# Kernel tuning notes

Hardware: AMD Instinct MI355X
Metric: run time of the kernel (lower is better)

The kernel has to match this reference:

```python
import jax, jax.numpy as jnp
import numpy as np

B, CIN, COUT, HID, K, H, W = 16, 512, 512, 512, 3, 64, 64

def setup_inputs() -> dict:
    key = jax.random.key(0)
    ks = jax.random.split(key, 8)
    x = jax.random.normal(ks[0], (B, CIN, H, W), dtype=jnp.float32)
    y = jax.random.normal(ks[1], (B, HID), dtype=jnp.float32)
    noise = jax.random.normal(ks[2], (B, 1, H, W), dtype=jnp.float32)
    # params (lrmul=1): weight ~ N(0,1)/sqrt(lrmul), bias zeros
    weight = jax.random.normal(ks[3], (COUT, CIN, K, K), dtype=jnp.float32)
    bias = jnp.zeros((1, COUT, 1, 1), dtype=jnp.float32)
    # ScaleLinear (equalized-lr linear): raw weight ~ N(0,1), runtime scale 1/sqrt(fan_in)
    mod_w = jax.random.normal(ks[4], (CIN, HID), dtype=jnp.float32)
    mod_b = jnp.zeros((CIN,), dtype=jnp.float32)
    noise_scale = jnp.zeros((1,), dtype=jnp.float32)
    return {"x": x, "y": y, "noise": noise, "weight": weight, "bias": bias,
            "mod_w": mod_w, "mod_b": mod_b, "noise_scale": noise_scale}

def reference(x, y, noise, weight, bias, mod_w, mod_b, noise_scale):
    O, I, k, _ = weight.shape
    runtime_coef = 1.0 / np.sqrt(I * k * k)  # gain=1, lrmul=1
    w = weight * runtime_coef                # shared scaled weight [O,I,k,k]
    # style modulation: s = mod(y) + 1, equalized-lr linear scale 1/sqrt(hidden)
    mod_scale = 1.0 / np.sqrt(mod_w.shape[1])
    s = y @ (mod_w.T * mod_scale) + mod_b + 1.0   # [B, I]
    # demodulation coeff without materializing per-sample weights:
    # d[b,o] = rsqrt(sum_{i,kx,ky} (w[o,i]*s[b,i])^2 + eps)
    w2 = jnp.sum(w * w, axis=(2, 3))              # [O, I]
    d = jax.lax.rsqrt(jnp.einsum('oi,bi->bo', w2, s * s) + 1e-8)  # [B, O]
    # fold modulation into input scale, demod into output scale (StyleGAN2 trick;
    # mathematically identical to grouped conv with per-sample weights)
    xm = x * s[:, :, None, None]
    out = jax.lax.conv_general_dilated(
        xm, w, window_strides=(1, 1), padding=((1, 1), (1, 1)),
        dimension_numbers=('NCHW', 'OIHW', 'NCHW'))
    out = out * d[:, :, None, None]
    out = out + noise * noise_scale   # noisy=True, explicit noise input
    out = out + bias                  # lrmul=1
    return out
```

## Files before the change

### kernel.cpp

```cpp
#include <hip/hip_runtime.h>
#include <hip/hip_bf16.h>

typedef unsigned short ushortT;
typedef __attribute__((ext_vector_type(8))) short short8;
typedef __attribute__((ext_vector_type(4))) float f32x4;

#define CIN 512
#define COUTC 512
#define HIDC 512
#define BATCH 16
#define HDIM 64
#define WDIM 64
#define HP 66


__device__ __forceinline__ unsigned short f2bf(float f) {
    __hip_bfloat16 h = __float2bfloat16(f);
    return __builtin_bit_cast(unsigned short, h);
}

__device__ __forceinline__ void gload16(const ushortT* g, ushortT* l) {
    __builtin_amdgcn_global_load_lds(
        (const __attribute__((address_space(1))) void*)g,
        (__attribute__((address_space(3))) void*)l, 16, 0, 0);
}

__global__ void k_style(const float* __restrict__ y, const float* __restrict__ mw,
                        const float* __restrict__ mb, float* __restrict__ s) {
    int lane = threadIdx.x & 63;
    int wid = blockIdx.x * 4 + (threadIdx.x >> 6);
    int b = wid >> 9, i = wid & 511;
    int h0 = lane * 8;
    float4 ya = *(const float4*)(y + b * HIDC + h0);
    float4 yb = *(const float4*)(y + b * HIDC + h0 + 4);
    float4 wa = *(const float4*)(mw + (size_t)i * HIDC + h0);
    float4 wb = *(const float4*)(mw + (size_t)i * HIDC + h0 + 4);
    float v = ya.x*wa.x + ya.y*wa.y + ya.z*wa.z + ya.w*wa.w
            + yb.x*wb.x + yb.y*wb.y + yb.z*wb.z + yb.w*wb.w;
    #pragma unroll
    for (int off = 32; off > 0; off >>= 1) v += __shfl_down(v, off);
    if (lane == 0) s[wid] = v * 0.04419417382415922f + mb[i] + 1.0f;
}

__global__ void k_prepw(const float* __restrict__ w, float* __restrict__ w2,
                        ushortT* __restrict__ wbt) {
    int t = blockIdx.x * 256 + threadIdx.x;
    const float* wp = w + (size_t)t * 9;
    const float coef = 0.014731391274719739f;
    float sum = 0.f;
    #pragma unroll
    for (int k = 0; k < 9; ++k) {
        float v = wp[k] * coef;
        sum += v * v;
        wbt[(size_t)k * (COUTC * CIN) + t] = f2bf(v);
    }
    w2[t] = sum;
}

__global__ void k_demod(const float* __restrict__ w2, const float* __restrict__ s,
                        float* __restrict__ d) {
    int lane = threadIdx.x & 63;
    int wid = blockIdx.x * 4 + (threadIdx.x >> 6);
    int b = wid >> 9, o = wid & 511;
    int i0 = lane * 8;
    float4 wa = *(const float4*)(w2 + (size_t)o * CIN + i0);
    float4 wb = *(const float4*)(w2 + (size_t)o * CIN + i0 + 4);
    float4 sa = *(const float4*)(s + b * CIN + i0);
    float4 sb = *(const float4*)(s + b * CIN + i0 + 4);
    float v = wa.x*sa.x*sa.x + wa.y*sa.y*sa.y + wa.z*sa.z*sa.z + wa.w*sa.w*sa.w
            + wb.x*sb.x*sb.x + wb.y*sb.y*sb.y + wb.z*sb.z*sb.z + wb.w*sb.w*sb.w;
    #pragma unroll
    for (int off = 32; off > 0; off >>= 1) v += __shfl_down(v, off);
    if (lane == 0) d[wid] = rsqrtf(v + 1e-8f);
}

__global__ void k_pad(const float* __restrict__ x, const float* __restrict__ s,
                      ushortT* __restrict__ xpad) {
    __shared__ float tilef[64 * 129];
    int bid = blockIdx.x;
    int cchunk = bid & 3;
    int rem = bid >> 2;
    int prow = rem % HP;
    int b = rem / HP;
    int tid = threadIdx.x;
    size_t rowbase = (((size_t)b * HP + prow) * HP) * CIN + cchunk * 128;
    if (prow == 0 || prow == HP - 1) {
        short8 z = {};
        for (int q = tid; q < HP * 16; q += 256) {
            int col = q >> 4, sub = q & 15;
            *(short8*)(xpad + rowbase + (size_t)col * CIN + sub * 8) = z;
        }
        return;
    }
    int xr = prow - 1;
    int u = tid & 15;
    int cbase = tid >> 4;
    #pragma unroll
    for (int it = 0; it < 8; ++it) {
        int c = cbase + it * 16;
        int ch = cchunk * 128 + c;
        float4 v = *(const float4*)(x + (((size_t)b * CIN + ch) * HDIM + xr) * WDIM + u * 4);
        float sv = s[b * CIN + ch];
        tilef[(u * 4 + 0) * 129 + c] = v.x * sv;
        tilef[(u * 4 + 1) * 129 + c] = v.y * sv;
        tilef[(u * 4 + 2) * 129 + c] = v.z * sv;
        tilef[(u * 4 + 3) * 129 + c] = v.w * sv;
    }
    __syncthreads();
    #pragma unroll
    for (int it = 0; it < 4; ++it) {
        int q = it * 256 + tid;
        int col = 1 + (q >> 4);
        int sub = q & 15;
        const float* tr = tilef + (col - 1) * 129 + sub * 8;
        short8 o;
        #pragma unroll
        for (int r = 0; r < 8; ++r) o[r] = (short)f2bf(tr[r]);
        *(short8*)(xpad + rowbase + (size_t)col * CIN + sub * 8) = o;
    }
    if (tid < 32) {
        short8 z = {};
        int bcol = (tid < 16) ? 0 : (HP - 1);
        *(short8*)(xpad + rowbase + (size_t)bcol * CIN + (tid & 15) * 8) = z;
    }
}

#define MFMA_CLUSTER(MH) do { \
    __builtin_amdgcn_s_setprio(1); \
    _Pragma("unroll") for (int m_ = 0; m_ < 4; ++m_) { \
        _Pragma("unroll") for (int n_ = 0; n_ < 4; ++n_) \
            acc[(MH)*4 + m_][n_] = __builtin_amdgcn_mfma_f32_16x16x32_bf16( \
                af[m_], bf[n_], acc[(MH)*4 + m_][n_], 0, 0, 0); } \
    __builtin_amdgcn_s_setprio(0); \
} while (0)

#define DS_A(MH, KH) do { \
    _Pragma("unroll") for (int m_ = 0; m_ < 4; ++m_) { \
        int row_ = wave_m * 128 + (MH)*64 + m_*16 + l15; \
        af[m_] = *(const short8*)(Ar + row_*64 + ((((KH)*4 + quad) ^ (row_ & 7)) * 8)); \
    } } while (0)

#define DS_B(KH) do { \
    _Pragma("unroll") for (int n_ = 0; n_ < 4; ++n_) { \
        int row_ = wave_n * 64 + n_*16 + l15; \
        bf[n_] = *(const short8*)(Br + row_*64 + ((((KH)*4 + quad) ^ (row_ & 7)) * 8)); \
    } } while (0)

__global__ __launch_bounds__(512, 2) void k_conv(
    const ushortT* __restrict__ wbt, const ushortT* __restrict__ xpad,
    const float* __restrict__ dcoef, const float* __restrict__ bias,
    const float* __restrict__ noise, const float* __restrict__ nscp,
    float* __restrict__ out)
{
    extern __shared__ __align__(16) ushortT smem[];

    int tid = threadIdx.x;
    int lane = tid & 63;
    int wave = tid >> 6;
    int wave_m = wave >> 2;
    int wave_n = wave & 3;
    int l15 = lane & 15;
    int quad = lane >> 4;

    int bid = blockIdx.x;
    int wg = (bid & 7) * 64 + (bid >> 3);
    int mtile = wg >> 8;
    int ntile = wg & 255;
    int b = ntile >> 4;
    int h0 = (ntile & 15) << 2;
    int cout0 = mtile << 8;

    unsigned aoff[4], boff[4], dstE[4];
    #pragma unroll
    for (int ca = 0; ca < 4; ++ca) {
        int a = ca * 512 + tid;
        int row = a >> 3;
        int sub = (a & 7) ^ (row & 7);
        aoff[ca] = (unsigned)((cout0 + row) * CIN + sub * 8);
        int prow = row >> 6;
        int pcol = row & 63;
        boff[ca] = (unsigned)((((b * HP) + h0 + prow) * HP + pcol) * CIN + sub * 8);
        dstE[ca] = (unsigned)(ca * 4096 + wave * 512);
    }

    f32x4 acc[8][4] = {};

    {
        const ushortT* Asrc = wbt;
        const ushortT* Bsrc = xpad;
        #pragma unroll
        for (int ca = 0; ca < 4; ++ca) {
            gload16(Asrc + aoff[ca], smem + dstE[ca]);
            gload16(Bsrc + boff[ca], smem + 32768 + dstE[ca]);
        }
        asm volatile("s_waitcnt vmcnt(0)" ::: "memory");
        __builtin_amdgcn_s_barrier();
    }

    #pragma unroll 2
    for (int ks = 0; ks < 72; ++ks) {
        int cur = ks & 1;
        const ushortT* Ar = smem + cur * 16384;
        const ushortT* Br = smem + 32768 + cur * 16384;
        ushortT* Aw = smem + (cur ^ 1) * 16384;
        ushortT* Bw = smem + 32768 + (cur ^ 1) * 16384;
        int ksn = ks + 1;
        bool st = ksn < 72;
        int tn = ksn >> 3, ccn = ksn & 7;
        const ushortT* Asrc = wbt + tn * (COUTC * CIN) + ccn * 64;
        const ushortT* Bsrc = xpad + ((tn / 3) * HP + (tn % 3)) * CIN + ccn * 64;

        short8 af[4], bf[4];

        if (st) {
            gload16(Asrc + aoff[0], Aw + dstE[0]); gload16(Bsrc + boff[0], Bw + dstE[0]);
            gload16(Asrc + aoff[1], Aw + dstE[1]); gload16(Bsrc + boff[1], Bw + dstE[1]);
        }
        DS_B(0);
        DS_A(0, 0);
        __builtin_amdgcn_s_barrier();
        asm volatile("s_waitcnt lgkmcnt(0)");
        MFMA_CLUSTER(0);
        __builtin_amdgcn_s_barrier();

        if (st) {
            gload16(Asrc + aoff[2], Aw + dstE[2]); gload16(Bsrc + boff[2], Bw + dstE[2]);
            gload16(Asrc + aoff[3], Aw + dstE[3]); gload16(Bsrc + boff[3], Bw + dstE[3]);
        }
        DS_A(1, 0);
        __builtin_amdgcn_s_barrier();
        asm volatile("s_waitcnt lgkmcnt(0)");
        MFMA_CLUSTER(1);
        __builtin_amdgcn_s_barrier();

        DS_B(1);
        DS_A(0, 1);
        __builtin_amdgcn_s_barrier();
        asm volatile("s_waitcnt lgkmcnt(0)");
        MFMA_CLUSTER(0);
        __builtin_amdgcn_s_barrier();

        DS_A(1, 1);
        __builtin_amdgcn_s_barrier();
        asm volatile("s_waitcnt lgkmcnt(0)");
        MFMA_CLUSTER(1);
        if (st) asm volatile("s_waitcnt vmcnt(0)");
        __builtin_amdgcn_s_barrier();
    }

    float ns = nscp[0];
    int col = lane & 15, rq = lane >> 4;
    #pragma unroll
    for (int nj = 0; nj < 4; ++nj) {
        int pos = wave_n * 64 + nj * 16 + col;
        int hh = h0 + (pos >> 6), ww = pos & 63;
        float nz = noise[((size_t)b << 12) + (hh << 6) + ww] * ns;
        #pragma unroll
        for (int mi = 0; mi < 8; ++mi) {
            int coutb = cout0 + wave_m * 128 + mi * 16 + rq * 4;
            f32x4 dv = *(const f32x4*)(dcoef + b * COUTC + coutb);
            f32x4 bv = *(const f32x4*)(bias + coutb);
            f32x4 a = acc[mi][nj];
            #pragma unroll
            for (int r = 0; r < 4; ++r) {
                out[(((size_t)(b * COUTC + coutb + r)) << 12) + (hh << 6) + ww]
                    = a[r] * dv[r] + nz + bv[r];
            }
        }
    }
}

extern "C" void kernel_launch(void* const* d_in, const int* in_sizes, int n_in,
                              void* d_out, int out_size, void* d_ws, size_t ws_size,
                              hipStream_t stream) {
    const float* x      = (const float*)d_in[0];
    const float* y      = (const float*)d_in[1];
    const float* noise  = (const float*)d_in[2];
    const float* weight = (const float*)d_in[3];
    const float* bias   = (const float*)d_in[4];
    const float* mod_w  = (const float*)d_in[5];
    const float* mod_b  = (const float*)d_in[6];
    const float* nsc    = (const float*)d_in[7];
    float* out = (float*)d_out;

    char* ws = (char*)d_ws;
    float*   s     = (float*)(ws);
    float*   dcoef = (float*)(ws + 32768);
    float*   w2    = (float*)(ws + 65536);
    ushortT* wbt   = (ushortT*)(ws + 1114112);
    ushortT* xpad  = (ushortT*)(ws + 5832704);

    static bool attr_done = false;
    if (!attr_done) {
        (void)hipFuncSetAttribute(reinterpret_cast<const void*>(k_conv),
                                  hipFuncAttributeMaxDynamicSharedMemorySize, 131072);
        attr_done = true;
    }

    k_style<<<dim3(2048), dim3(256), 0, stream>>>(y, mod_w, mod_b, s);
    k_prepw<<<dim3(1024), dim3(256), 0, stream>>>(weight, w2, wbt);
    k_demod<<<dim3(2048), dim3(256), 0, stream>>>(w2, s, dcoef);
    k_pad<<<dim3(BATCH * HP * 4), dim3(256), 0, stream>>>(x, s, xpad);
    k_conv<<<dim3(512), dim3(512), 131072, stream>>>(wbt, xpad, dcoef, bias, noise, nsc, out);
}
```

Measured before the change: 532.7 us.

## Switch conv main loop to 4-stage pipeline with BK=32 and deeper prefetch

```diff
diff --git a/kernel.cpp b/kernel.cpp
--- a/kernel.cpp
+++ b/kernel.cpp
@@ -12,6 +12,7 @@
 #define HDIM 64
 #define WDIM 64
 #define HP 66
+#define NSTEP 144
 
 
 __device__ __forceinline__ unsigned short f2bf(float f) {
@@ -125,7 +126,7 @@
     }
 }
 
-#define MFMA_CLUSTER(MH) do { \
+#define CLUST(MH) do { \
     __builtin_amdgcn_s_setprio(1); \
     _Pragma("unroll") for (int m_ = 0; m_ < 4; ++m_) { \
         _Pragma("unroll") for (int n_ = 0; n_ < 4; ++n_) \
@@ -134,17 +135,29 @@
     __builtin_amdgcn_s_setprio(0); \
 } while (0)
 
-#define DS_A(MH, KH) do { \
+#define DS_A(MH, Abase) do { \
     _Pragma("unroll") for (int m_ = 0; m_ < 4; ++m_) { \
         int row_ = wave_m * 128 + (MH)*64 + m_*16 + l15; \
-        af[m_] = *(const short8*)(Ar + row_*64 + ((((KH)*4 + quad) ^ (row_ & 7)) * 8)); \
+        af[m_] = *(const short8*)((Abase) + row_*32 + ((quad ^ ((row_ >> 2) & 3)) * 8)); \
     } } while (0)
 
-#define DS_B(KH) do { \
+#define DS_B(Bbase) do { \
     _Pragma("unroll") for (int n_ = 0; n_ < 4; ++n_) { \
         int row_ = wave_n * 64 + n_*16 + l15; \
-        bf[n_] = *(const short8*)(Br + row_*64 + ((((KH)*4 + quad) ^ (row_ & 7)) * 8)); \
+        bf[n_] = *(const short8*)((Bbase) + row_*32 + ((quad ^ ((row_ >> 2) & 3)) * 8)); \
     } } while (0)
+
+#define STAGE(KSN) do { \
+    int tn_ = (KSN) >> 4, ccn_ = (KSN) & 15; \
+    const ushortT* As_ = wbt + (size_t)tn_ * (COUTC * CIN) + ccn_ * 32; \
+    const ushortT* Bs_ = xpad + ((size_t)(tn_ / 3) * HP + (tn_ % 3)) * CIN + ccn_ * 32; \
+    ushortT* Ad_ = smem + ((KSN) & 3) * 8192; \
+    ushortT* Bd_ = smem + 32768 + ((KSN) & 3) * 8192; \
+    gload16(As_ + aoff[0], Ad_ + dstE[0]); \
+    gload16(As_ + aoff[1], Ad_ + dstE[1]); \
+    gload16(Bs_ + boff[0], Bd_ + dstE[0]); \
+    gload16(Bs_ + boff[1], Bd_ + dstE[1]); \
+} while (0)
 
 __global__ __launch_bounds__(512, 2) void k_conv(
     const ushortT* __restrict__ wbt, const ushortT* __restrict__ xpad,
@@ -170,12 +183,12 @@
     int h0 = (ntile & 15) << 2;
     int cout0 = mtile << 8;
 
-    unsigned aoff[4], boff[4], dstE[4];
-    #pragma unroll
-    for (int ca = 0; ca < 4; ++ca) {
+    unsigned aoff[2], boff[2], dstE[2];
+    #pragma unroll
+    for (int ca = 0; ca < 2; ++ca) {
         int a = ca * 512 + tid;
-        int row = a >> 3;
-        int sub = (a & 7) ^ (row & 7);
+        int row = a >> 2;
+        int sub = (a & 3) ^ ((row >> 2) & 3);
         aoff[ca] = (unsigned)((cout0 + row) * CIN + sub * 8);
         int prow = row >> 6;
         int pcol = row & 63;
@@ -185,67 +198,39 @@
 
     f32x4 acc[8][4] = {};
 
-    {
-        const ushortT* Asrc = wbt;
-        const ushortT* Bsrc = xpad;
-        #pragma unroll
-        for (int ca = 0; ca < 4; ++ca) {
-            gload16(Asrc + aoff[ca], smem + dstE[ca]);
-            gload16(Bsrc + boff[ca], smem + 32768 + dstE[ca]);
+    STAGE(0);
+    STAGE(1);
+    STAGE(2);
+    asm volatile("s_waitcnt vmcnt(8)" ::: "memory");
+    __builtin_amdgcn_s_barrier();
+
+    #pragma unroll 4
+    for (int ks = 0; ks < NSTEP; ++ks) {
+        int buf = ks & 3;
+        const ushortT* Abuf = smem + buf * 8192;
+        const ushortT* Bbuf = smem + 32768 + buf * 8192;
+        int ksn = ks + 3;
+
+        short8 af[4], bf[4];
+
+        if (ksn < NSTEP) STAGE(ksn);
+        DS_B(Bbuf);
+        DS_A(0, Abuf);
+        __builtin_amdgcn_s_barrier();
+        asm volatile("s_waitcnt lgkmcnt(0)" ::: "memory");
+        CLUST(0);
+        __builtin_amdgcn_s_barrier();
+
+        DS_A(1, Abuf);
+        __builtin_amdgcn_s_barrier();
+        asm volatile("s_waitcnt lgkmcnt(0)" ::: "memory");
+        CLUST(1);
+        if (ks + 1 < NSTEP) {
+            if (ksn < NSTEP)          asm volatile("s_waitcnt vmcnt(8)" ::: "memory");
+            else if (ks + 2 < NSTEP)  asm volatile("s_waitcnt vmcnt(4)" ::: "memory");
+            else                      asm volatile("s_waitcnt vmcnt(0)" ::: "memory");
+            __builtin_amdgcn_s_barrier();
         }
-        asm volatile("s_waitcnt vmcnt(0)" ::: "memory");
-        __builtin_amdgcn_s_barrier();
-    }
-
-    #pragma unroll 2
-    for (int ks = 0; ks < 72; ++ks) {
-        int cur = ks & 1;
-        const ushortT* Ar = smem + cur * 16384;
-        const ushortT* Br = smem + 32768 + cur * 16384;
-        ushortT* Aw = smem + (cur ^ 1) * 16384;
-        ushortT* Bw = smem + 32768 + (cur ^ 1) * 16384;
-        int ksn = ks + 1;
-        bool st = ksn < 72;
-        int tn = ksn >> 3, ccn = ksn & 7;
-        const ushortT* Asrc = wbt + tn * (COUTC * CIN) + ccn * 64;
-        const ushortT* Bsrc = xpad + ((tn / 3) * HP + (tn % 3)) * CIN + ccn * 64;
-
-        short8 af[4], bf[4];
-
-        if (st) {
-            gload16(Asrc + aoff[0], Aw + dstE[0]); gload16(Bsrc + boff[0], Bw + dstE[0]);
-            gload16(Asrc + aoff[1], Aw + dstE[1]); gload16(Bsrc + boff[1], Bw + dstE[1]);
-        }
-        DS_B(0);
-        DS_A(0, 0);
-        __builtin_amdgcn_s_barrier();
-        asm volatile("s_waitcnt lgkmcnt(0)");
-        MFMA_CLUSTER(0);
-        __builtin_amdgcn_s_barrier();
-
-        if (st) {
-            gload16(Asrc + aoff[2], Aw + dstE[2]); gload16(Bsrc + boff[2], Bw + dstE[2]);
-            gload16(Asrc + aoff[3], Aw + dstE[3]); gload16(Bsrc + boff[3], Bw + dstE[3]);
-        }
-        DS_A(1, 0);
-        __builtin_amdgcn_s_barrier();
-        asm volatile("s_waitcnt lgkmcnt(0)");
-        MFMA_CLUSTER(1);
-        __builtin_amdgcn_s_barrier();
-
-        DS_B(1);
-        DS_A(0, 1);
-        __builtin_amdgcn_s_barrier();
-        asm volatile("s_waitcnt lgkmcnt(0)");
-        MFMA_CLUSTER(0);
-        __builtin_amdgcn_s_barrier();
-
-        DS_A(1, 1);
-        __builtin_amdgcn_s_barrier();
-        asm volatile("s_waitcnt lgkmcnt(0)");
-        MFMA_CLUSTER(1);
-        if (st) asm volatile("s_waitcnt vmcnt(0)");
-        __builtin_amdgcn_s_barrier();
     }
 
     float ns = nscp[0];
```

Result: no change. 541.7 us (+1.7%).
